# Performance work log

Hardware: AMD Instinct MI355X
Metric: run time of the kernel (lower is better)

## Reference

```python
import jax, jax.numpy as jnp
import numpy as np

B, N, D, NS, ITERS = 16, 4096, 512, 16, 3
EPS = 1e-8
H = max(D, 128)  # hidden_dim = max(dim, hidden_dim)
SCALE = D ** -0.5
LN_EPS = 1e-5  # torch LayerNorm default


def _ln(x, g, b):
    mu = x.mean(-1, keepdims=True)
    var = ((x - mu) ** 2).mean(-1, keepdims=True)
    return (x - mu) / jnp.sqrt(var + LN_EPS) * g + b


def setup_inputs() -> dict:
    key = jax.random.key(0)
    ks = jax.random.split(key, 16)
    s = 0.02
    return {
        "inputs": jax.random.normal(ks[0], (B, N, D), jnp.float32),
        "q_inp": jax.random.normal(ks[1], (B, N, D), jnp.float32),
        "k_inp": jax.random.normal(ks[2], (B, N, D), jnp.float32),
        "v_inp": jax.random.normal(ks[3], (B, N, D), jnp.float32),
        "slots_mu": jax.random.normal(ks[4], (1, NS, D), jnp.float32),
        "prompts": jax.random.uniform(ks[5], (1, NS, D), jnp.float32),
        "Wq": jax.random.normal(ks[6], (D, D), jnp.float32) * s,
        "bq": jnp.zeros((D,), jnp.float32),
        "W_ih": jax.random.normal(ks[7], (3 * D, D), jnp.float32) * s,
        "b_ih": jnp.zeros((3 * D,), jnp.float32),
        "W_hh": jax.random.normal(ks[8], (3 * D, D), jnp.float32) * s,
        "b_hh": jnp.zeros((3 * D,), jnp.float32),
        "W1": jax.random.normal(ks[9], (H, D), jnp.float32) * s,
        "b1": jnp.zeros((H,), jnp.float32),
        "W2": jax.random.normal(ks[10], (D, H), jnp.float32) * s,
        "b2": jnp.zeros((D,), jnp.float32),
        "gk": jnp.ones((D,), jnp.float32), "bk": jnp.zeros((D,), jnp.float32),
        "gv": jnp.ones((D,), jnp.float32), "bv": jnp.zeros((D,), jnp.float32),
        "gs": jnp.ones((D,), jnp.float32), "bs": jnp.zeros((D,), jnp.float32),
        "gff": jnp.ones((D,), jnp.float32), "bff": jnp.zeros((D,), jnp.float32),
    }


def reference(inputs, q_inp, k_inp, v_inp, slots_mu, prompts, Wq, bq,
              W_ih, b_ih, W_hh, b_hh, W1, b1, W2, b2,
              gk, bk, gv, bv, gs, bs, gff, bff):
    b = inputs.shape[0]
    slots = jnp.broadcast_to(slots_mu, (b, NS, D))
    prm = jnp.broadcast_to(prompts, (b, NS, D))
    k = _ln(k_inp, gk, bk)
    v = _ln(v_inp, gv, bv)

    attn = None
    for _ in range(ITERS):
        slots_prev = slots
        s = _ln(slots, gs, bs)
        q = jnp.einsum('bnd,ed->bne', s, Wq) + bq
        dots = jnp.einsum('bid,bjd->bij', q, k) * SCALE
        attn = jax.nn.softmax(dots, axis=1) + EPS  # inverted softmax over slots
        attn_n = attn / attn.sum(-1, keepdims=True)
        updates = jnp.einsum('bjd,bij->bid', v, attn_n)
        # GRUCell (torch semantics: gates order r, z, n)
        x = updates.reshape(-1, D)
        h = slots_prev.reshape(-1, D)
        gx = x @ W_ih.T + b_ih
        gh = h @ W_hh.T + b_hh
        rx, zx, nx = jnp.split(gx, 3, axis=-1)
        rh, zh, nh = jnp.split(gh, 3, axis=-1)
        r = jax.nn.sigmoid(rx + rh)
        z = jax.nn.sigmoid(zx + zh)
        n_t = jnp.tanh(nx + r * nh)
        slots = ((1.0 - z) * n_t + z * h).reshape(b, NS, D)
        ff = _ln(slots, gff, bff)
        slots = slots + (jax.nn.relu(ff @ W1.T + b1) @ W2.T + b2)

    # torch: einsum('bnd,bnp->bdp', ...).permute(0,2,1) == 'bnd,bnp->bpd'
    prompt_feature = jnp.einsum('bnd,bnp->bpd', prm, attn)
    slot_feature = jnp.einsum('bnd,bnp->bpd', slots, attn)
    return (slots, attn, prompt_feature, slot_feature, slot_feature)
```

## Files before the change

### kernel.cpp

```cpp
#include <hip/hip_runtime.h>
#include <math.h>

#define NN 4096
#define DD 512
#define NSL 16
#define SCALE_F 0.044194173824159216f
#define LN_EPS_F 1e-5f
#define ATTN_EPS_F 1e-8f

typedef float4 f4;
typedef __fp16 h2 __attribute__((ext_vector_type(2)));
typedef _Float16 h2f __attribute__((ext_vector_type(2)));
typedef _Float16 h8 __attribute__((ext_vector_type(8)));
typedef float f32x4 __attribute__((ext_vector_type(4)));

__device__ __forceinline__ float dot4f(f4 a, f4 b){
    return a.x*b.x + a.y*b.y + a.z*b.z + a.w*b.w;
}
__device__ __forceinline__ float fdot2u(unsigned a, unsigned b, float c){
    return __builtin_amdgcn_fdot2(__builtin_bit_cast(h2f, a),
                                  __builtin_bit_cast(h2f, b), c, false);
}
__device__ __forceinline__ unsigned pk(float x, float y){
    return __builtin_bit_cast(unsigned, __builtin_amdgcn_cvt_pkrtz(x, y));
}

__global__ __launch_bounds__(256) void k_prep(const float* __restrict__ mu,
        const float* __restrict__ kin, const float* __restrict__ vin,
        float* __restrict__ slots, __fp16* __restrict__ slotsh,
        float* __restrict__ kmu, float* __restrict__ krstd,
        float* __restrict__ vmu, float* __restrict__ vrstd,
        __fp16* __restrict__ kh, __fp16* __restrict__ vh,
        const float* __restrict__ Wq, const float* __restrict__ Wih,
        const float* __restrict__ Whh, const float* __restrict__ W1,
        const float* __restrict__ W2,
        uint2* __restrict__ TWq, uint2* __restrict__ TWih, uint2* __restrict__ TWhh,
        uint2* __restrict__ TW1, uint2* __restrict__ TW2){
    int bx = blockIdx.x, t = threadIdx.x;
    int gid = bx*256 + t;
    if (bx < 128){
        int idx = gid;
        f4 v = ((const f4*)mu)[idx & 2047];
        ((f4*)slots)[idx] = v;
        uint2 o; o.x = pk(v.x, v.y); o.y = pk(v.z, v.w);
        ((uint2*)slotsh)[idx] = o;
    }
    int sub = t & 15;
    int rl  = t >> 4;
#pragma unroll
    for (int pass = 0; pass < 8; pass++){
        int task = bx*128 + pass*16 + rl;
        int half = task >> 16;
        int row  = task & 65535;
        const float* src = half ? kin : vin;
        __fp16* dsth = half ? kh : vh;
        const f4* r4 = (const f4*)(src + (size_t)row*DD);
        uint2* w2 = (uint2*)(dsth + (size_t)row*DD);
        float s = 0.f, ss = 0.f;
#pragma unroll
        for (int k2 = 0; k2 < 8; k2++){
            f4 x = r4[sub + k2*16];
            s  += x.x+x.y+x.z+x.w;
            ss += x.x*x.x+x.y*x.y+x.z*x.z+x.w*x.w;
            uint2 o; o.x = pk(x.x, x.y); o.y = pk(x.z, x.w);
            w2[sub + k2*16] = o;
        }
        for (int o = 1; o < 16; o <<= 1){
            s += __shfl_xor(s, o); ss += __shfl_xor(ss, o);
        }
        if (sub == 0){
            float m = s*(1.f/DD);
            float rs = rsqrtf(ss*(1.f/DD) - m*m + LN_EPS_F);
            if (half){ kmu[row] = m; krstd[row] = rs; }
            else     { vmu[row] = m; vrstd[row] = rs; }
        }
    }
    for (int id = gid; id < 589824; id += 262144){
        const float* W; uint2* TW; int R, local;
        if (id < 65536)      { W = Wq;  TW = TWq;  R = 512;  local = id; }
        else if (id < 262144){ W = Wih; TW = TWih; R = 1536; local = id - 65536; }
        else if (id < 458752){ W = Whh; TW = TWhh; R = 1536; local = id - 262144; }
        else if (id < 524288){ W = W1;  TW = TW1;  R = 512;  local = id - 458752; }
        else                 { W = W2;  TW = TW2;  R = 512;  local = id - 524288; }
        int kk = local / R, c = local - kk*R;
        f4 w = ((const f4*)W)[(size_t)c*128 + kk];
        uint2 o; o.x = pk(w.x, w.y); o.y = pk(w.z, w.w);
        TW[local] = o;
    }
}

__global__ __launch_bounds__(256) void k_ln_q(const float* __restrict__ slots,
        const float* __restrict__ gs, const float* __restrict__ bs,
        const uint2* __restrict__ TWq, const float* __restrict__ bq,
        const float* __restrict__ gk, const float* __restrict__ bk,
        __fp16* __restrict__ qgh, float* __restrict__ C1p, float* __restrict__ C2p){
    __shared__ uint2 rowh[4][128];
    int lane = threadIdx.x & 63, wv = threadIdx.x >> 6;
    int m = blockIdx.y*4 + wv;
    int c = blockIdx.x*64 + lane;
    const f4* r4 = (const f4*)(slots + (size_t)m*DD);
    f4 v0 = r4[lane*2], v1 = r4[lane*2+1];
    float s  = v0.x+v0.y+v0.z+v0.w + v1.x+v1.y+v1.z+v1.w;
    float ss = v0.x*v0.x+v0.y*v0.y+v0.z*v0.z+v0.w*v0.w
             + v1.x*v1.x+v1.y*v1.y+v1.z*v1.z+v1.w*v1.w;
    for (int o = 32; o; o >>= 1){ s += __shfl_down(s,o); ss += __shfl_down(ss,o); }
    s = __shfl(s,0); ss = __shfl(ss,0);
    float mu = s*(1.f/DD);
    float rstd = rsqrtf(ss*(1.f/DD) - mu*mu + LN_EPS_F);
    const f4* g4 = (const f4*)gs; const f4* b4 = (const f4*)bs;
    f4 g0 = g4[lane*2], g1 = g4[lane*2+1], c0 = b4[lane*2], c1 = b4[lane*2+1];
    f4 o0, o1;
    o0.x=(v0.x-mu)*rstd*g0.x+c0.x; o0.y=(v0.y-mu)*rstd*g0.y+c0.y;
    o0.z=(v0.z-mu)*rstd*g0.z+c0.z; o0.w=(v0.w-mu)*rstd*g0.w+c0.w;
    o1.x=(v1.x-mu)*rstd*g1.x+c1.x; o1.y=(v1.y-mu)*rstd*g1.y+c1.y;
    o1.z=(v1.z-mu)*rstd*g1.z+c1.z; o1.w=(v1.w-mu)*rstd*g1.w+c1.w;
    rowh[wv][lane*2]     = uint2{pk(o0.x,o0.y), pk(o0.z,o0.w)};
    rowh[wv][lane*2 + 1] = uint2{pk(o1.x,o1.y), pk(o1.z,o1.w)};
    __syncthreads();
    float acc = 0.f;
    for (int kk = 0; kk < 128; kk++){
        uint2 q2 = rowh[wv][kk];
        uint2 w2 = TWq[(size_t)kk*512 + c];
        acc = fdot2u(w2.x, q2.x, acc);
        acc = fdot2u(w2.y, q2.y, acc);
    }
    float q0 = acc + bq[c];
    float qg0 = q0 * gk[c];
    float qg1 = __shfl_down(qg0, 1);
    if (!(lane & 1))
        ((unsigned*)qgh)[(size_t)m*256 + (c>>1)] = pk(qg0, qg1);
    float r1 = qg0, r2 = q0 * bk[c];
    for (int o = 32; o; o >>= 1){ r1 += __shfl_down(r1,o); r2 += __shfl_down(r2,o); }
    if (lane == 0){
        C1p[blockIdx.x*256 + m] = r1;
        C2p[blockIdx.x*256 + m] = r2;
    }
}

__global__ __launch_bounds__(256, 4) void k_attn_av(const __fp16* __restrict__ kh,
        const __fp16* __restrict__ vh, const __fp16* __restrict__ qgh,
        const float* __restrict__ C1p, const float* __restrict__ C2p,
        const float* __restrict__ kmu, const float* __restrict__ krstd,
        const float* __restrict__ vmu, const float* __restrict__ vrstd,
        float* __restrict__ Sp, float* __restrict__ Mp, __fp16* __restrict__ Uwp,
        float* __restrict__ attn_out, int last){
    __shared__ __align__(16) unsigned qLr[16*260];
    __shared__ __align__(16) unsigned wLp[32*20];
    __shared__ float c1s[NSL], c2s[NSL];
    __shared__ float kmuL[64], krsL[64], vmuL[64], vrsL[64];
    __shared__ float spL[4][NSL], mpL[4][NSL];
    int chunk = blockIdx.x, b = blockIdx.y;
    int t = threadIdx.x, lane = t & 63, wv = t >> 6;

    const unsigned* qsrc = (const unsigned*)(qgh + (size_t)b*NSL*DD);
    for (int e = t; e < 4096; e += 256)
        qLr[(e >> 8)*260 + (e & 255)] = qsrc[e];
    if (t < NSL){
        float c1 = 0.f, c2 = 0.f;
#pragma unroll
        for (int k = 0; k < 8; k++){
            c1 += C1p[k*256 + b*NSL + t];
            c2 += C2p[k*256 + b*NSL + t];
        }
        c1s[t] = c1; c2s[t] = c2;
    }
    {
        int grp = t >> 6, j0 = t & 63;
        size_t gidx = (size_t)b*NN + chunk*64 + j0;
        if (grp == 0) kmuL[j0] = kmu[gidx];
        else if (grp == 1) krsL[j0] = krstd[gidx];
        else if (grp == 2) vmuL[j0] = vmu[gidx];
        else vrsL[j0] = vrstd[gidx];
    }
    __syncthreads();

    int i = lane & 15, g = lane >> 4;
    int jbase = chunk*64 + wv*16;
    const uint4* ka = (const uint4*)(kh + ((size_t)b*NN + jbase + i)*DD);
    const uint4* qb4 = (const uint4*)qLr;
    f32x4 acc = {0.f, 0.f, 0.f, 0.f};
#pragma unroll
    for (int ks = 0; ks < 16; ks++){
        uint4 af = ka[ks*4 + g];
        uint4 bf = qb4[i*65 + ks*4 + g];
        acc = __builtin_amdgcn_mfma_f32_16x16x32_f16(
                  __builtin_bit_cast(h8, af), __builtin_bit_cast(h8, bf), acc, 0, 0, 0);
    }
    float c1i = c1s[i], c2i = c2s[i];
    float a4[4], w4v[4];
    float S_part = 0.f, M_part = 0.f;
#pragma unroll
    for (int r = 0; r < 4; r++){
        int jl = g*4 + r;
        float mu = kmuL[wv*16 + jl], rstd = krsL[wv*16 + jl];
        float dv = SCALE_F*(rstd*(acc[r] - mu*c1i) + c2i);
        float mx = dv;
        mx = fmaxf(mx, __shfl_xor(mx, 1));
        mx = fmaxf(mx, __shfl_xor(mx, 2));
        mx = fmaxf(mx, __shfl_xor(mx, 4));
        mx = fmaxf(mx, __shfl_xor(mx, 8));
        float e = __expf(dv - mx);
        float se = e;
        se += __shfl_xor(se, 1);
        se += __shfl_xor(se, 2);
        se += __shfl_xor(se, 4);
        se += __shfl_xor(se, 8);
        float a = e/se + ATTN_EPS_F;
        a4[r] = a;
        float rv = vrsL[wv*16 + jl], vm = vmuL[wv*16 + jl];
        w4v[r] = a*rv;
        S_part += a;
        M_part += a*rv*vm;
    }
    wLp[(wv*8 + g*2)*20 + i]     = pk(w4v[0], w4v[1]);
    wLp[(wv*8 + g*2 + 1)*20 + i] = pk(w4v[2], w4v[3]);
    S_part += __shfl_xor(S_part, 16);
    S_part += __shfl_xor(S_part, 32);
    M_part += __shfl_xor(M_part, 16);
    M_part += __shfl_xor(M_part, 32);
    if (lane < 16){ spL[wv][lane] = S_part; mpL[wv][lane] = M_part; }
    if (last){
#pragma unroll
        for (int r = 0; r < 4; r++)
            attn_out[((size_t)b*NSL + i)*NN + jbase + g*4 + r] = a4[r];
    }
    __syncthreads();

    if (t < NSL)
        Sp[((size_t)b*NSL + t)*64 + chunk] = spL[0][t]+spL[1][t]+spL[2][t]+spL[3][t];
    else if (t < 2*NSL){
        int ii = t - NSL;
        Mp[((size_t)b*NSL + ii)*64 + chunk] = mpL[0][ii]+mpL[1][ii]+mpL[2][ii]+mpL[3][ii];
    }

    f4 ax[4], ay[4];
#pragma unroll
    for (int g2 = 0; g2 < 4; g2++){ ax[g2] = f4{0,0,0,0}; ay[g2] = f4{0,0,0,0}; }
    const unsigned* v2h = (const unsigned*)(vh + ((size_t)b*NN + (size_t)chunk*64)*DD);
#pragma unroll 2
    for (int p = 0; p < 32; p++){
        unsigned vu0 = v2h[(size_t)(2*p)*256 + t];
        unsigned vu1 = v2h[(size_t)(2*p+1)*256 + t];
        unsigned pd0 = __builtin_amdgcn_perm(vu1, vu0, 0x05040100u);
        unsigned pd1 = __builtin_amdgcn_perm(vu1, vu0, 0x07060302u);
        const uint4* wp4 = (const uint4*)(wLp + p*20);
#pragma unroll
        for (int g2 = 0; g2 < 4; g2++){
            uint4 w = wp4[g2];
            ax[g2].x = fdot2u(w.x, pd0, ax[g2].x);
            ax[g2].y = fdot2u(w.y, pd0, ax[g2].y);
            ax[g2].z = fdot2u(w.z, pd0, ax[g2].z);
            ax[g2].w = fdot2u(w.w, pd0, ax[g2].w);
            ay[g2].x = fdot2u(w.x, pd1, ay[g2].x);
            ay[g2].y = fdot2u(w.y, pd1, ay[g2].y);
            ay[g2].z = fdot2u(w.z, pd1, ay[g2].z);
            ay[g2].w = fdot2u(w.w, pd1, ay[g2].w);
        }
    }
#pragma unroll
    for (int g2 = 0; g2 < 4; g2++){
        const float* px = (const float*)&ax[g2];
        const float* py = (const float*)&ay[g2];
#pragma unroll
        for (int c4 = 0; c4 < 4; c4++){
            int ii = g2*4 + c4;
            ((unsigned*)Uwp)[(((size_t)(b*NSL + ii))*64 + chunk)*256 + t] = pk(px[c4], py[c4]);
        }
    }
}

__global__ __launch_bounds__(256) void k_upd(const __fp16* __restrict__ Uwp,
        const float* __restrict__ Sp, const float* __restrict__ Mp,
        const float* __restrict__ gv, const float* __restrict__ bv,
        __fp16* __restrict__ updh){
    __shared__ float sm[2];
    int m = blockIdx.x, t = threadIdx.x;
    if (t < 128){
        float val = (t < 64) ? Sp[(size_t)m*64 + (t&63)] : Mp[(size_t)m*64 + (t&63)];
        for (int o = 1; o < 64; o <<= 1) val += __shfl_xor(val, o);
        if (t == 0)  sm[0] = val;
        if (t == 64) sm[1] = val;
    }
    __syncthreads();
    float Sv = sm[0], Mv = sm[1];
    float rS = 1.f/Sv;
    float accx = 0.f, accy = 0.f;
    const unsigned* base = (const unsigned*)Uwp + (size_t)m*64*256 + t;
#pragma unroll 8
    for (int ch = 0; ch < 64; ch++){
        h2 u = __builtin_bit_cast(h2, base[(size_t)ch*256]);
        accx += (float)u.x; accy += (float)u.y;
    }
    float2 gvv = ((const float2*)gv)[t];
    float2 bvv = ((const float2*)bv)[t];
    float ox = gvv.x*(accx - Mv)*rS + bvv.x;
    float oy = gvv.y*(accy - Mv)*rS + bvv.y;
    ((unsigned*)updh)[(size_t)m*256 + t] = pk(ox, oy);
}

__global__ __launch_bounds__(256) void k_gru_mm(const __fp16* __restrict__ xh, const __fp16* __restrict__ hh,
        const uint2* __restrict__ TWih, const float* __restrict__ bih,
        const uint2* __restrict__ TWhh, const float* __restrict__ bhh,
        float* __restrict__ gpA, float* __restrict__ gpB){
    int lane = threadIdx.x & 63, wv = threadIdx.x >> 6;
    int c = blockIdx.x*64 + lane;
    int m0 = blockIdx.y*16 + wv*4;
    int ks = blockIdx.z;
    int k0 = ks*64, k1 = k0 + 64;
    float* gp = ks ? gpB : gpA;
    int type = c >> 9;
    const uint2* x2 = (const uint2*)xh;
    const uint2* h2_ = (const uint2*)hh;
    float acc[4] = {0,0,0,0};
    float bias;
    if (type <= 1){
#pragma unroll 2
        for (int kk = k0; kk < k1; kk++){
            uint2 wa = TWih[(size_t)kk*1536 + c];
            uint2 wb = TWhh[(size_t)kk*1536 + c];
#pragma unroll
            for (int mm = 0; mm < 4; mm++){
                uint2 xa = x2[(size_t)(m0+mm)*128 + kk];
                uint2 ha = h2_[(size_t)(m0+mm)*128 + kk];
                acc[mm] = fdot2u(wa.x, xa.x, acc[mm]);
                acc[mm] = fdot2u(wa.y, xa.y, acc[mm]);
                acc[mm] = fdot2u(wb.x, ha.x, acc[mm]);
                acc[mm] = fdot2u(wb.y, ha.y, acc[mm]);
            }
        }
        bias = bih[c] + bhh[c];
    } else if (type == 2){
#pragma unroll 2
        for (int kk = k0; kk < k1; kk++){
            uint2 wa = TWih[(size_t)kk*1536 + c];
#pragma unroll
            for (int mm = 0; mm < 4; mm++){
                uint2 xa = x2[(size_t)(m0+mm)*128 + kk];
                acc[mm] = fdot2u(wa.x, xa.x, acc[mm]);
                acc[mm] = fdot2u(wa.y, xa.y, acc[mm]);
            }
        }
        bias = bih[c];
    } else {
        int cr = c - 512;
#pragma unroll 2
        for (int kk = k0; kk < k1; kk++){
            uint2 wb = TWhh[(size_t)kk*1536 + cr];
#pragma unroll
            for (int mm = 0; mm < 4; mm++){
                uint2 ha = h2_[(size_t)(m0+mm)*128 + kk];
                acc[mm] = fdot2u(wb.x, ha.x, acc[mm]);
                acc[mm] = fdot2u(wb.y, ha.y, acc[mm]);
            }
        }
        bias = bhh[cr];
    }
    float bout = ks ? 0.f : bias;
#pragma unroll
    for (int mm = 0; mm < 4; mm++)
        gp[(size_t)(m0+mm)*2048 + c] = acc[mm] + bout;
}

__global__ __launch_bounds__(256) void k_tail1(const float* __restrict__ gpA,
        const float* __restrict__ gpB, const float* __restrict__ slots,
        const float* __restrict__ gff, const float* __restrict__ bff,
        const uint2* __restrict__ TW1, const float* __restrict__ b1,
        float* __restrict__ slots2, __fp16* __restrict__ hidh){
    __shared__ uint2 rowh[4][128];
    int lane = threadIdx.x & 63, wv = threadIdx.x >> 6;
    int m = blockIdx.y*4 + wv;
    int c = blockIdx.x*64 + lane;
    const f4* g0 = (const f4*)(gpA + (size_t)m*2048);
    const f4* g1 = (const f4*)(gpB + (size_t)m*2048);
    const f4* h4 = (const f4*)(slots + (size_t)m*DD);
    f4 s2v[2];
    float s = 0.f, ss = 0.f;
#pragma unroll
    for (int half = 0; half < 2; half++){
        int e = lane*2 + half;
        f4 rp = g0[e],      zp = g0[128+e],  nx = g0[256+e],  nh = g0[384+e];
        f4 rq = g1[e],      zq = g1[128+e],  ny = g1[256+e],  nz = g1[384+e];
        rp.x+=rq.x; rp.y+=rq.y; rp.z+=rq.z; rp.w+=rq.w;
        zp.x+=zq.x; zp.y+=zq.y; zp.z+=zq.z; zp.w+=zq.w;
        nx.x+=ny.x; nx.y+=ny.y; nx.z+=ny.z; nx.w+=ny.w;
        nh.x+=nz.x; nh.y+=nz.y; nh.z+=nz.z; nh.w+=nz.w;
        f4 hv = h4[e];
        f4 o;
        {
            float r = 1.f/(1.f + __expf(-rp.x));
            float z = 1.f/(1.f + __expf(-zp.x));
            float n = tanhf(nx.x + r*nh.x);
            o.x = (1.f - z)*n + z*hv.x;
            r = 1.f/(1.f + __expf(-rp.y)); z = 1.f/(1.f + __expf(-zp.y));
            n = tanhf(nx.y + r*nh.y);
            o.y = (1.f - z)*n + z*hv.y;
            r = 1.f/(1.f + __expf(-rp.z)); z = 1.f/(1.f + __expf(-zp.z));
            n = tanhf(nx.z + r*nh.z);
            o.z = (1.f - z)*n + z*hv.z;
            r = 1.f/(1.f + __expf(-rp.w)); z = 1.f/(1.f + __expf(-zp.w));
            n = tanhf(nx.w + r*nh.w);
            o.w = (1.f - z)*n + z*hv.w;
        }
        s2v[half] = o;
        s  += o.x+o.y+o.z+o.w;
        ss += o.x*o.x+o.y*o.y+o.z*o.z+o.w*o.w;
        if (blockIdx.x == 0)
            ((f4*)(slots2 + (size_t)m*DD))[e] = o;
    }
    for (int o = 32; o; o >>= 1){ s += __shfl_down(s,o); ss += __shfl_down(ss,o); }
    s = __shfl(s,0); ss = __shfl(ss,0);
    float mu = s*(1.f/DD);
    float rstd = rsqrtf(ss*(1.f/DD) - mu*mu + LN_EPS_F);
    const f4* gg4 = (const f4*)gff; const f4* bb4 = (const f4*)bff;
#pragma unroll
    for (int half = 0; half < 2; half++){
        int e = lane*2 + half;
        f4 gg = gg4[e], bb = bb4[e], o = s2v[half], n;
        n.x = (o.x-mu)*rstd*gg.x + bb.x;
        n.y = (o.y-mu)*rstd*gg.y + bb.y;
        n.z = (o.z-mu)*rstd*gg.z + bb.z;
        n.w = (o.w-mu)*rstd*gg.w + bb.w;
        rowh[wv][e] = uint2{pk(n.x,n.y), pk(n.z,n.w)};
    }
    __syncthreads();
    float acc = 0.f;
    for (int kk = 0; kk < 128; kk++){
        uint2 q2 = rowh[wv][kk];
        uint2 w2 = TW1[(size_t)kk*512 + c];
        acc = fdot2u(w2.x, q2.x, acc);
        acc = fdot2u(w2.y, q2.y, acc);
    }
    float hv = fmaxf(acc + b1[c], 0.f);
    hidh[(size_t)m*DD + c] = (__fp16)hv;
}

__global__ __launch_bounds__(256) void k_ffn2(const __fp16* __restrict__ hidh, const uint2* __restrict__ TW2,
                                              const float* __restrict__ b2, const float* __restrict__ slots2,
                                              float* __restrict__ slots, __fp16* __restrict__ slotsh,
                                              float* __restrict__ out_slots, int last){
    int lane = threadIdx.x & 63, wv = threadIdx.x >> 6;
    int d = blockIdx.x*64 + lane;
    int m = blockIdx.y*4 + wv;
    const uint2* h2_ = (const uint2*)(hidh + (size_t)m*DD);
    float acc = 0.f;
    for (int kk = 0; kk < 128; kk++){
        uint2 hh = h2_[kk];
        uint2 w2 = TW2[(size_t)kk*512 + d];
        acc = fdot2u(w2.x, hh.x, acc);
        acc = fdot2u(w2.y, hh.y, acc);
    }
    float v0 = slots2[(size_t)m*DD + d] + acc + b2[d];
    slots[(size_t)m*DD + d] = v0;
    slotsh[(size_t)m*DD + d] = (__fp16)v0;
    if (last) out_slots[(size_t)m*DD + d] = v0;
}

__global__ __launch_bounds__(256) void k_features(const float* __restrict__ prompts, const float* __restrict__ slots,
        const float* __restrict__ attn, float* __restrict__ pf, float* __restrict__ sf, float* __restrict__ sf2){
    int b = blockIdx.y;
    int pbase = blockIdx.x*32;
    int t = threadIdx.x;
    __shared__ float al[NSL][33];
    for (int idx = t; idx < NSL*32; idx += 256){
        int i = idx >> 5, pp = idx & 31;
        al[i][pp] = attn[((size_t)b*NSL + i)*NN + pbase + pp];
    }
    float2 pr[NSL], sl[NSL];
    const float2* p2 = (const float2*)prompts;
    const float2* s2 = (const float2*)(slots + (size_t)b*NSL*DD);
#pragma unroll
    for (int i = 0; i < NSL; i++){ pr[i] = p2[i*256+t]; sl[i] = s2[i*256+t]; }
    __syncthreads();
    for (int pp = 0; pp < 32; pp++){
        float a0=0.f, a1=0.f, c0=0.f, c1=0.f;
#pragma unroll
        for (int i = 0; i < NSL; i++){
            float a = al[i][pp];
            a0 += a*pr[i].x; a1 += a*pr[i].y;
            c0 += a*sl[i].x; c1 += a*sl[i].y;
        }
        size_t o = ((size_t)b*NN + pbase + pp)*DD + 2*t;
        float2 pv; pv.x=a0; pv.y=a1;
        float2 sv; sv.x=c0; sv.y=c1;
        *(float2*)(pf + o)  = pv;
        *(float2*)(sf + o)  = sv;
        *(float2*)(sf2 + o) = sv;
    }
}

extern "C" void kernel_launch(void* const* d_in, const int* in_sizes, int n_in,
                              void* d_out, int out_size, void* d_ws, size_t ws_size,
                              hipStream_t stream) {
    const float* k_inp   = (const float*)d_in[2];
    const float* v_inp   = (const float*)d_in[3];
    const float* slots_mu= (const float*)d_in[4];
    const float* prompts = (const float*)d_in[5];
    const float* Wq      = (const float*)d_in[6];
    const float* bq      = (const float*)d_in[7];
    const float* W_ih    = (const float*)d_in[8];
    const float* b_ih    = (const float*)d_in[9];
    const float* W_hh    = (const float*)d_in[10];
    const float* b_hh    = (const float*)d_in[11];
    const float* W1      = (const float*)d_in[12];
    const float* b1      = (const float*)d_in[13];
    const float* W2      = (const float*)d_in[14];
    const float* b2      = (const float*)d_in[15];
    const float* gk      = (const float*)d_in[16];
    const float* bk      = (const float*)d_in[17];
    const float* gv      = (const float*)d_in[18];
    const float* bv      = (const float*)d_in[19];
    const float* gs      = (const float*)d_in[20];
    const float* bs      = (const float*)d_in[21];
    const float* gff     = (const float*)d_in[22];
    const float* bff     = (const float*)d_in[23];

    float* ws = (float*)d_ws;
    float* slots   = ws + 0;
    float* slots2  = ws + 131072;
    float* gp      = ws + 262144;
    float* C1p     = ws + 786432;
    float* C2p     = ws + 788480;
    float* kmu     = ws + 790528;
    float* krstd   = ws + 856064;
    float* vmu     = ws + 921600;
    float* vrstd   = ws + 987136;
    float* Sp      = ws + 1052672;
    float* Mp      = ws + 1069056;
    __fp16* slotsh = (__fp16*)(ws + 1085440);
    __fp16* updh   = (__fp16*)(ws + 1150976);
    __fp16* hidh   = (__fp16*)(ws + 1216512);
    __fp16* qgh    = (__fp16*)(ws + 1282048);
    uint2* TWqh  = (uint2*)(ws + 1347584);
    uint2* TWihh = (uint2*)(ws + 1478656);
    uint2* TWhhh = (uint2*)(ws + 1871872);
    uint2* TW1h  = (uint2*)(ws + 2265088);
    uint2* TW2h  = (uint2*)(ws + 2396160);

    float* out      = (float*)d_out;
    float* attn_out = out + 131072;
    float* pf       = out + 1179648;
    float* sf       = pf + 33554432;
    float* sf2      = sf + 33554432;
    __fp16* Uwp     = (__fp16*)pf;
    float* gpB      = pf + 16777216;
    __fp16* kh      = (__fp16*)sf;
    __fp16* vh      = (__fp16*)sf2;

    k_prep<<<1024, 256, 0, stream>>>(slots_mu, k_inp, v_inp, slots, slotsh,
                                     kmu, krstd, vmu, vrstd, kh, vh,
                                     Wq, W_ih, W_hh, W1, W2,
                                     TWqh, TWihh, TWhhh, TW1h, TW2h);

    for (int it = 0; it < 3; it++){
        int last = (it == 2);
        k_ln_q<<<dim3(8,64), 256, 0, stream>>>(slots, gs, bs, TWqh, bq, gk, bk, qgh, C1p, C2p);
        k_attn_av<<<dim3(64,16), 256, 0, stream>>>(kh, vh, qgh, C1p, C2p,
                                                   kmu, krstd, vmu, vrstd,
                                                   Sp, Mp, Uwp, attn_out, last);
        k_upd<<<256, 256, 0, stream>>>(Uwp, Sp, Mp, gv, bv, updh);
        k_gru_mm<<<dim3(32,16,2), 256, 0, stream>>>(updh, slotsh, TWihh, b_ih, TWhhh, b_hh, gp, gpB);
        k_tail1<<<dim3(8,64), 256, 0, stream>>>(gp, gpB, slots, gff, bff, TW1h, b1, slots2, hidh);
        k_ffn2<<<dim3(8,64), 256, 0, stream>>>(hidh, TW2h, b2, slots2, slots, slotsh, out, last);
    }

    k_features<<<dim3(128,16), 256, 0, stream>>>(prompts, slots, attn_out, pf, sf, sf2);
}
```

Before: 558.3 us.

## Fuse GRU tail, FFN and next-iteration LN+Q projection into one kernel

Merges k_tail1, k_ffn2 and the following iteration's k_ln_q into a single per-slot-row kernel with 512 threads. Intermediates (normalized rows, hidden activations) stay in LDS, and the slots2/hidh round trips through global memory go away. The first iteration's query is computed once from slots_mu by a small kernel and broadcast to all batches. This saves launches per iteration, but each block now runs three serial 512-wide matvecs over only 256 blocks, which lowers parallelism.

```diff
diff --git a/kernel.cpp b/kernel.cpp
--- a/kernel.cpp
+++ b/kernel.cpp
@@ -89,57 +89,52 @@
     }
 }
 
-__global__ __launch_bounds__(256) void k_ln_q(const float* __restrict__ slots,
+__global__ __launch_bounds__(256) void k_q0(const float* __restrict__ mu_,
+        const float* __restrict__ Wq, const float* __restrict__ bq,
         const float* __restrict__ gs, const float* __restrict__ bs,
-        const uint2* __restrict__ TWq, const float* __restrict__ bq,
         const float* __restrict__ gk, const float* __restrict__ bk,
-        __fp16* __restrict__ qgh, float* __restrict__ C1p, float* __restrict__ C2p){
-    __shared__ uint2 rowh[4][128];
-    int lane = threadIdx.x & 63, wv = threadIdx.x >> 6;
-    int m = blockIdx.y*4 + wv;
-    int c = blockIdx.x*64 + lane;
-    const f4* r4 = (const f4*)(slots + (size_t)m*DD);
-    f4 v0 = r4[lane*2], v1 = r4[lane*2+1];
-    float s  = v0.x+v0.y+v0.z+v0.w + v1.x+v1.y+v1.z+v1.w;
-    float ss = v0.x*v0.x+v0.y*v0.y+v0.z*v0.z+v0.w*v0.w
-             + v1.x*v1.x+v1.y*v1.y+v1.z*v1.z+v1.w*v1.w;
+        __fp16* __restrict__ qgh, float* __restrict__ C1v, float* __restrict__ C2v){
+    __shared__ __align__(16) float rowF[512];
+    __shared__ float sm[16];
+    int i = blockIdx.x, t = threadIdx.x, lane = t & 63, wv = t >> 6;
+    float2 x = ((const float2*)(mu_ + (size_t)i*DD))[t];
+    float s = x.x + x.y, ss = x.x*x.x + x.y*x.y;
     for (int o = 32; o; o >>= 1){ s += __shfl_down(s,o); ss += __shfl_down(ss,o); }
-    s = __shfl(s,0); ss = __shfl(ss,0);
-    float mu = s*(1.f/DD);
-    float rstd = rsqrtf(ss*(1.f/DD) - mu*mu + LN_EPS_F);
-    const f4* g4 = (const f4*)gs; const f4* b4 = (const f4*)bs;
-    f4 g0 = g4[lane*2], g1 = g4[lane*2+1], c0 = b4[lane*2], c1 = b4[lane*2+1];
-    f4 o0, o1;
-    o0.x=(v0.x-mu)*rstd*g0.x+c0.x; o0.y=(v0.y-mu)*rstd*g0.y+c0.y;
-    o0.z=(v0.z-mu)*rstd*g0.z+c0.z; o0.w=(v0.w-mu)*rstd*g0.w+c0.w;
-    o1.x=(v1.x-mu)*rstd*g1.x+c1.x; o1.y=(v1.y-mu)*rstd*g1.y+c1.y;
-    o1.z=(v1.z-mu)*rstd*g1.z+c1.z; o1.w=(v1.w-mu)*rstd*g1.w+c1.w;
-    rowh[wv][lane*2]     = uint2{pk(o0.x,o0.y), pk(o0.z,o0.w)};
-    rowh[wv][lane*2 + 1] = uint2{pk(o1.x,o1.y), pk(o1.z,o1.w)};
-    __syncthreads();
-    float acc = 0.f;
-    for (int kk = 0; kk < 128; kk++){
-        uint2 q2 = rowh[wv][kk];
-        uint2 w2 = TWq[(size_t)kk*512 + c];
-        acc = fdot2u(w2.x, q2.x, acc);
-        acc = fdot2u(w2.y, q2.y, acc);
-    }
-    float q0 = acc + bq[c];
-    float qg0 = q0 * gk[c];
-    float qg1 = __shfl_down(qg0, 1);
-    if (!(lane & 1))
-        ((unsigned*)qgh)[(size_t)m*256 + (c>>1)] = pk(qg0, qg1);
-    float r1 = qg0, r2 = q0 * bk[c];
-    for (int o = 32; o; o >>= 1){ r1 += __shfl_down(r1,o); r2 += __shfl_down(r2,o); }
-    if (lane == 0){
-        C1p[blockIdx.x*256 + m] = r1;
-        C2p[blockIdx.x*256 + m] = r2;
+    if (lane == 0){ sm[wv] = s; sm[8+wv] = ss; }
+    __syncthreads();
+    s = sm[0]+sm[1]+sm[2]+sm[3]; ss = sm[8]+sm[9]+sm[10]+sm[11];
+    float mu = s*(1.f/DD), rstd = rsqrtf(ss*(1.f/DD) - mu*mu + LN_EPS_F);
+    rowF[2*t]   = (x.x-mu)*rstd*gs[2*t]   + bs[2*t];
+    rowF[2*t+1] = (x.y-mu)*rstd*gs[2*t+1] + bs[2*t+1];
+    __syncthreads();
+    float c1p = 0.f, c2p = 0.f;
+#pragma unroll
+    for (int rep = 0; rep < 2; rep++){
+        int c = t + rep*256;
+        const f4* wrow = (const f4*)(Wq + (size_t)c*DD);
+        const f4* rf = (const f4*)rowF;
+        float acc = 0.f;
+        for (int k = 0; k < 128; k++) acc += dot4f(rf[k], wrow[k]);
+        float q0 = acc + bq[c];
+        float qg = q0 * gk[c];
+        __fp16 qh = (__fp16)qg;
+        for (int b = 0; b < 16; b++)
+            qgh[((size_t)(b*16+i))*DD + c] = qh;
+        c1p += qg; c2p += q0*bk[c];
+    }
+    for (int o = 32; o; o >>= 1){ c1p += __shfl_down(c1p,o); c2p += __shfl_down(c2p,o); }
+    if (lane == 0){ sm[wv] = c1p; sm[8+wv] = c2p; }
+    __syncthreads();
+    if (t == 0){
+        float r1 = sm[0]+sm[1]+sm[2]+sm[3];
+        float r2 = sm[8]+sm[9]+sm[10]+sm[11];
+        for (int b = 0; b < 16; b++){ C1v[b*16+i] = r1; C2v[b*16+i] = r2; }
     }
 }
 
 __global__ __launch_bounds__(256, 4) void k_attn_av(const __fp16* __restrict__ kh,
         const __fp16* __restrict__ vh, const __fp16* __restrict__ qgh,
-        const float* __restrict__ C1p, const float* __restrict__ C2p,
+        const float* __restrict__ C1v, const float* __restrict__ C2v,
         const float* __restrict__ kmu, const float* __restrict__ krstd,
         const float* __restrict__ vmu, const float* __restrict__ vrstd,
         float* __restrict__ Sp, float* __restrict__ Mp, __fp16* __restrict__ Uwp,
@@ -155,15 +150,7 @@
     const unsigned* qsrc = (const unsigned*)(qgh + (size_t)b*NSL*DD);
     for (int e = t; e < 4096; e += 256)
         qLr[(e >> 8)*260 + (e & 255)] = qsrc[e];
-    if (t < NSL){
-        float c1 = 0.f, c2 = 0.f;
-#pragma unroll
-        for (int k = 0; k < 8; k++){
-            c1 += C1p[k*256 + b*NSL + t];
-            c2 += C2p[k*256 + b*NSL + t];
-        }
-        c1s[t] = c1; c2s[t] = c2;
-    }
+    if (t < NSL){ c1s[t] = C1v[b*NSL + t]; c2s[t] = C2v[b*NSL + t]; }
     {
         int grp = t >> 6, j0 = t & 63;
         size_t gidx = (size_t)b*NN + chunk*64 + j0;
@@ -361,98 +348,99 @@
         gp[(size_t)(m0+mm)*2048 + c] = acc[mm] + bout;
 }
 
-__global__ __launch_bounds__(256) void k_tail1(const float* __restrict__ gpA,
-        const float* __restrict__ gpB, const float* __restrict__ slots,
+__global__ __launch_bounds__(512) void k_tail(const float* __restrict__ gpA,
+        const float* __restrict__ gpB, float* __restrict__ slots,
         const float* __restrict__ gff, const float* __restrict__ bff,
         const uint2* __restrict__ TW1, const float* __restrict__ b1,
-        float* __restrict__ slots2, __fp16* __restrict__ hidh){
-    __shared__ uint2 rowh[4][128];
-    int lane = threadIdx.x & 63, wv = threadIdx.x >> 6;
-    int m = blockIdx.y*4 + wv;
-    int c = blockIdx.x*64 + lane;
-    const f4* g0 = (const f4*)(gpA + (size_t)m*2048);
-    const f4* g1 = (const f4*)(gpB + (size_t)m*2048);
-    const f4* h4 = (const f4*)(slots + (size_t)m*DD);
-    f4 s2v[2];
-    float s = 0.f, ss = 0.f;
-#pragma unroll
-    for (int half = 0; half < 2; half++){
-        int e = lane*2 + half;
-        f4 rp = g0[e],      zp = g0[128+e],  nx = g0[256+e],  nh = g0[384+e];
-        f4 rq = g1[e],      zq = g1[128+e],  ny = g1[256+e],  nz = g1[384+e];
-        rp.x+=rq.x; rp.y+=rq.y; rp.z+=rq.z; rp.w+=rq.w;
-        zp.x+=zq.x; zp.y+=zq.y; zp.z+=zq.z; zp.w+=zq.w;
-        nx.x+=ny.x; nx.y+=ny.y; nx.z+=ny.z; nx.w+=ny.w;
-        nh.x+=nz.x; nh.y+=nz.y; nh.z+=nz.z; nh.w+=nz.w;
-        f4 hv = h4[e];
-        f4 o;
-        {
-            float r = 1.f/(1.f + __expf(-rp.x));
-            float z = 1.f/(1.f + __expf(-zp.x));
-            float n = tanhf(nx.x + r*nh.x);
-            o.x = (1.f - z)*n + z*hv.x;
-            r = 1.f/(1.f + __expf(-rp.y)); z = 1.f/(1.f + __expf(-zp.y));
-            n = tanhf(nx.y + r*nh.y);
-            o.y = (1.f - z)*n + z*hv.y;
-            r = 1.f/(1.f + __expf(-rp.z)); z = 1.f/(1.f + __expf(-zp.z));
-            n = tanhf(nx.z + r*nh.z);
-            o.z = (1.f - z)*n + z*hv.z;
-            r = 1.f/(1.f + __expf(-rp.w)); z = 1.f/(1.f + __expf(-zp.w));
-            n = tanhf(nx.w + r*nh.w);
-            o.w = (1.f - z)*n + z*hv.w;
-        }
-        s2v[half] = o;
-        s  += o.x+o.y+o.z+o.w;
-        ss += o.x*o.x+o.y*o.y+o.z*o.z+o.w*o.w;
-        if (blockIdx.x == 0)
-            ((f4*)(slots2 + (size_t)m*DD))[e] = o;
-    }
+        const uint2* __restrict__ TW2, const float* __restrict__ b2,
+        const float* __restrict__ gs, const float* __restrict__ bs,
+        const uint2* __restrict__ TWq, const float* __restrict__ bq,
+        const float* __restrict__ gk, const float* __restrict__ bk,
+        __fp16* __restrict__ slotsh, __fp16* __restrict__ qgh,
+        float* __restrict__ C1v, float* __restrict__ C2v,
+        float* __restrict__ out_slots, int last){
+    __shared__ __align__(8) __fp16 rowL[512];
+    __shared__ __align__(8) __fp16 hidL[512];
+    __shared__ float sm[16];
+    int m = blockIdx.x, t = threadIdx.x;
+    int lane = t & 63, wv = t >> 6;
+    const float* g0 = gpA + (size_t)m*2048;
+    const float* g1 = gpB + (size_t)m*2048;
+    float rp  = g0[t]       + g1[t];
+    float zp  = g0[512+t]   + g1[512+t];
+    float nx  = g0[1024+t]  + g1[1024+t];
+    float nh_ = g0[1536+t]  + g1[1536+t];
+    float h = slots[(size_t)m*DD + t];
+    float r = 1.f/(1.f + __expf(-rp));
+    float z = 1.f/(1.f + __expf(-zp));
+    float n = tanhf(nx + r*nh_);
+    float s2 = (1.f - z)*n + z*h;
+    float s = s2, ss = s2*s2;
     for (int o = 32; o; o >>= 1){ s += __shfl_down(s,o); ss += __shfl_down(ss,o); }
-    s = __shfl(s,0); ss = __shfl(ss,0);
-    float mu = s*(1.f/DD);
-    float rstd = rsqrtf(ss*(1.f/DD) - mu*mu + LN_EPS_F);
-    const f4* gg4 = (const f4*)gff; const f4* bb4 = (const f4*)bff;
-#pragma unroll
-    for (int half = 0; half < 2; half++){
-        int e = lane*2 + half;
-        f4 gg = gg4[e], bb = bb4[e], o = s2v[half], n;
-        n.x = (o.x-mu)*rstd*gg.x + bb.x;
-        n.y = (o.y-mu)*rstd*gg.y + bb.y;
-        n.z = (o.z-mu)*rstd*gg.z + bb.z;
-        n.w = (o.w-mu)*rstd*gg.w + bb.w;
-        rowh[wv][e] = uint2{pk(n.x,n.y), pk(n.z,n.w)};
-    }
-    __syncthreads();
+    if (lane == 0){ sm[wv] = s; sm[8+wv] = ss; }
+    __syncthreads();
+    s  = sm[0]+sm[1]+sm[2]+sm[3]+sm[4]+sm[5]+sm[6]+sm[7];
+    ss = sm[8]+sm[9]+sm[10]+sm[11]+sm[12]+sm[13]+sm[14]+sm[15];
+    float mu = s*(1.f/DD), rstd = rsqrtf(ss*(1.f/DD) - mu*mu + LN_EPS_F);
+    __syncthreads();
+    rowL[t] = (__fp16)((s2-mu)*rstd*gff[t] + bff[t]);
+    __syncthreads();
+    const uint2* ffv = (const uint2*)rowL;
     float acc = 0.f;
+#pragma unroll 4
     for (int kk = 0; kk < 128; kk++){
-        uint2 q2 = rowh[wv][kk];
-        uint2 w2 = TW1[(size_t)kk*512 + c];
-        acc = fdot2u(w2.x, q2.x, acc);
-        acc = fdot2u(w2.y, q2.y, acc);
-    }
-    float hv = fmaxf(acc + b1[c], 0.f);
-    hidh[(size_t)m*DD + c] = (__fp16)hv;
-}
-
-__global__ __launch_bounds__(256) void k_ffn2(const __fp16* __restrict__ hidh, const uint2* __restrict__ TW2,
-                                              const float* __restrict__ b2, const float* __restrict__ slots2,
-                                              float* __restrict__ slots, __fp16* __restrict__ slotsh,
-                                              float* __restrict__ out_slots, int last){
-    int lane = threadIdx.x & 63, wv = threadIdx.x >> 6;
-    int d = blockIdx.x*64 + lane;
-    int m = blockIdx.y*4 + wv;
-    const uint2* h2_ = (const uint2*)(hidh + (size_t)m*DD);
-    float acc = 0.f;
+        uint2 w = TW1[(size_t)kk*512 + t];
+        uint2 q = ffv[kk];
+        acc = fdot2u(w.x, q.x, acc);
+        acc = fdot2u(w.y, q.y, acc);
+    }
+    hidL[t] = (__fp16)fmaxf(acc + b1[t], 0.f);
+    __syncthreads();
+    const uint2* hv = (const uint2*)hidL;
+    float acc2 = 0.f;
+#pragma unroll 4
     for (int kk = 0; kk < 128; kk++){
-        uint2 hh = h2_[kk];
-        uint2 w2 = TW2[(size_t)kk*512 + d];
-        acc = fdot2u(w2.x, hh.x, acc);
-        acc = fdot2u(w2.y, hh.y, acc);
-    }
-    float v0 = slots2[(size_t)m*DD + d] + acc + b2[d];
-    slots[(size_t)m*DD + d] = v0;
-    slotsh[(size_t)m*DD + d] = (__fp16)v0;
-    if (last) out_slots[(size_t)m*DD + d] = v0;
+        uint2 w = TW2[(size_t)kk*512 + t];
+        uint2 q = hv[kk];
+        acc2 = fdot2u(w.x, q.x, acc2);
+        acc2 = fdot2u(w.y, q.y, acc2);
+    }
+    float v0 = s2 + acc2 + b2[t];
+    slots[(size_t)m*DD + t] = v0;
+    slotsh[(size_t)m*DD + t] = (__fp16)v0;
+    if (last){
+        out_slots[(size_t)m*DD + t] = v0;
+        return;
+    }
+    float s3 = v0, ss3 = v0*v0;
+    for (int o = 32; o; o >>= 1){ s3 += __shfl_down(s3,o); ss3 += __shfl_down(ss3,o); }
+    if (lane == 0){ sm[wv] = s3; sm[8+wv] = ss3; }
+    __syncthreads();
+    s3  = sm[0]+sm[1]+sm[2]+sm[3]+sm[4]+sm[5]+sm[6]+sm[7];
+    ss3 = sm[8]+sm[9]+sm[10]+sm[11]+sm[12]+sm[13]+sm[14]+sm[15];
+    float mu2 = s3*(1.f/DD), rstd2 = rsqrtf(ss3*(1.f/DD) - mu2*mu2 + LN_EPS_F);
+    __syncthreads();
+    rowL[t] = (__fp16)((v0-mu2)*rstd2*gs[t] + bs[t]);
+    __syncthreads();
+    float accq = 0.f;
+#pragma unroll 4
+    for (int kk = 0; kk < 128; kk++){
+        uint2 w = TWq[(size_t)kk*512 + t];
+        uint2 q = ffv[kk];
+        accq = fdot2u(w.x, q.x, accq);
+        accq = fdot2u(w.y, q.y, accq);
+    }
+    float q0 = accq + bq[t];
+    float qg = q0 * gk[t];
+    qgh[(size_t)m*DD + t] = (__fp16)qg;
+    float c1 = qg, c2 = q0*bk[t];
+    for (int o = 32; o; o >>= 1){ c1 += __shfl_down(c1,o); c2 += __shfl_down(c2,o); }
+    if (lane == 0){ sm[wv] = c1; sm[8+wv] = c2; }
+    __syncthreads();
+    if (t == 0){
+        C1v[m] = sm[0]+sm[1]+sm[2]+sm[3]+sm[4]+sm[5]+sm[6]+sm[7];
+        C2v[m] = sm[8]+sm[9]+sm[10]+sm[11]+sm[12]+sm[13]+sm[14]+sm[15];
+    }
 }
 
 __global__ __launch_bounds__(256) void k_features(const float* __restrict__ prompts, const float* __restrict__ slots,
@@ -516,25 +504,23 @@
 
     float* ws = (float*)d_ws;
     float* slots   = ws + 0;
-    float* slots2  = ws + 131072;
-    float* gp      = ws + 262144;
-    float* C1p     = ws + 786432;
-    float* C2p     = ws + 788480;
-    float* kmu     = ws + 790528;
-    float* krstd   = ws + 856064;
-    float* vmu     = ws + 921600;
-    float* vrstd   = ws + 987136;
-    float* Sp      = ws + 1052672;
-    float* Mp      = ws + 1069056;
-    __fp16* slotsh = (__fp16*)(ws + 1085440);
-    __fp16* updh   = (__fp16*)(ws + 1150976);
-    __fp16* hidh   = (__fp16*)(ws + 1216512);
-    __fp16* qgh    = (__fp16*)(ws + 1282048);
-    uint2* TWqh  = (uint2*)(ws + 1347584);
-    uint2* TWihh = (uint2*)(ws + 1478656);
-    uint2* TWhhh = (uint2*)(ws + 1871872);
-    uint2* TW1h  = (uint2*)(ws + 2265088);
-    uint2* TW2h  = (uint2*)(ws + 2396160);
+    float* gp      = ws + 131072;
+    float* C1v     = ws + 655360;
+    float* C2v     = ws + 655616;
+    float* kmu     = ws + 655872;
+    float* krstd   = ws + 721408;
+    float* vmu     = ws + 786944;
+    float* vrstd   = ws + 852480;
+    float* Sp      = ws + 918016;
+    float* Mp      = ws + 934400;
+    __fp16* slotsh = (__fp16*)(ws + 950784);
+    __fp16* updh   = (__fp16*)(ws + 1016320);
+    __fp16* qgh    = (__fp16*)(ws + 1081856);
+    uint2* TWqh  = (uint2*)(ws + 1147392);
+    uint2* TWihh = (uint2*)(ws + 1278464);
+    uint2* TWhhh = (uint2*)(ws + 1671680);
+    uint2* TW1h  = (uint2*)(ws + 2064896);
+    uint2* TW2h  = (uint2*)(ws + 2195968);
 
     float* out      = (float*)d_out;
     float* attn_out = out + 131072;
@@ -550,17 +536,18 @@
                                      kmu, krstd, vmu, vrstd, kh, vh,
                                      Wq, W_ih, W_hh, W1, W2,
                                      TWqh, TWihh, TWhhh, TW1h, TW2h);
+    k_q0<<<16, 256, 0, stream>>>(slots_mu, Wq, bq, gs, bs, gk, bk, qgh, C1v, C2v);
 
     for (int it = 0; it < 3; it++){
         int last = (it == 2);
-        k_ln_q<<<dim3(8,64), 256, 0, stream>>>(slots, gs, bs, TWqh, bq, gk, bk, qgh, C1p, C2p);
-        k_attn_av<<<dim3(64,16), 256, 0, stream>>>(kh, vh, qgh, C1p, C2p,
+        k_attn_av<<<dim3(64,16), 256, 0, stream>>>(kh, vh, qgh, C1v, C2v,
                                                    kmu, krstd, vmu, vrstd,
                                                    Sp, Mp, Uwp, attn_out, last);
         k_upd<<<256, 256, 0, stream>>>(Uwp, Sp, Mp, gv, bv, updh);
         k_gru_mm<<<dim3(32,16,2), 256, 0, stream>>>(updh, slotsh, TWihh, b_ih, TWhhh, b_hh, gp, gpB);
-        k_tail1<<<dim3(8,64), 256, 0, stream>>>(gp, gpB, slots, gff, bff, TW1h, b1, slots2, hidh);
-        k_ffn2<<<dim3(8,64), 256, 0, stream>>>(hidh, TW2h, b2, slots2, slots, slotsh, out, last);
+        k_tail<<<256, 512, 0, stream>>>(gp, gpB, slots, gff, bff, TW1h, b1, TW2h, b2,
+                                        gs, bs, TWqh, bq, gk, bk,
+                                        slotsh, qgh, C1v, C2v, out, last);
     }
 
     k_features<<<dim3(128,16), 256, 0, stream>>>(prompts, slots, attn_out, pf, sf, sf2);
```

Measured after the change: 576.6 us. +3.3%, slower.

## Fuse slot LayerNorm and q projection into FFN2 tail kernel

Applied to the files above, without the earlier changes.

Removes the separate per-iteration LN+q kernel. The first-iteration q is now computed once from slots_mu, which is identical across batches, and broadcast to all batches. Later iterations compute q inside the FFN2 kernel, so each block recomputes the full 512-wide FFN2 row to get LayerNorm statistics before doing its 64-column q slice. This saves a launch and a global round-trip per iteration but makes each FFN2 block do eight times the FFN2 matvec work.

```diff
diff --git a/kernel.cpp b/kernel.cpp
--- a/kernel.cpp
+++ b/kernel.cpp
@@ -89,51 +89,53 @@
     }
 }
 
-__global__ __launch_bounds__(256) void k_ln_q(const float* __restrict__ slots,
+__global__ __launch_bounds__(256) void k_q0(const float* __restrict__ mu_,
+        const float* __restrict__ Wq, const float* __restrict__ bq,
         const float* __restrict__ gs, const float* __restrict__ bs,
-        const uint2* __restrict__ TWq, const float* __restrict__ bq,
         const float* __restrict__ gk, const float* __restrict__ bk,
         __fp16* __restrict__ qgh, float* __restrict__ C1p, float* __restrict__ C2p){
-    __shared__ uint2 rowh[4][128];
-    int lane = threadIdx.x & 63, wv = threadIdx.x >> 6;
-    int m = blockIdx.y*4 + wv;
-    int c = blockIdx.x*64 + lane;
-    const f4* r4 = (const f4*)(slots + (size_t)m*DD);
-    f4 v0 = r4[lane*2], v1 = r4[lane*2+1];
-    float s  = v0.x+v0.y+v0.z+v0.w + v1.x+v1.y+v1.z+v1.w;
-    float ss = v0.x*v0.x+v0.y*v0.y+v0.z*v0.z+v0.w*v0.w
-             + v1.x*v1.x+v1.y*v1.y+v1.z*v1.z+v1.w*v1.w;
+    __shared__ __align__(16) float rowF[512];
+    __shared__ float sm[16];
+    int i = blockIdx.x, t = threadIdx.x, lane = t & 63, wv = t >> 6;
+    float2 x = ((const float2*)(mu_ + (size_t)i*DD))[t];
+    float s = x.x + x.y, ss = x.x*x.x + x.y*x.y;
     for (int o = 32; o; o >>= 1){ s += __shfl_down(s,o); ss += __shfl_down(ss,o); }
-    s = __shfl(s,0); ss = __shfl(ss,0);
-    float mu = s*(1.f/DD);
-    float rstd = rsqrtf(ss*(1.f/DD) - mu*mu + LN_EPS_F);
-    const f4* g4 = (const f4*)gs; const f4* b4 = (const f4*)bs;
-    f4 g0 = g4[lane*2], g1 = g4[lane*2+1], c0 = b4[lane*2], c1 = b4[lane*2+1];
-    f4 o0, o1;
-    o0.x=(v0.x-mu)*rstd*g0.x+c0.x; o0.y=(v0.y-mu)*rstd*g0.y+c0.y;
-    o0.z=(v0.z-mu)*rstd*g0.z+c0.z; o0.w=(v0.w-mu)*rstd*g0.w+c0.w;
-    o1.x=(v1.x-mu)*rstd*g1.x+c1.x; o1.y=(v1.y-mu)*rstd*g1.y+c1.y;
-    o1.z=(v1.z-mu)*rstd*g1.z+c1.z; o1.w=(v1.w-mu)*rstd*g1.w+c1.w;
-    rowh[wv][lane*2]     = uint2{pk(o0.x,o0.y), pk(o0.z,o0.w)};
-    rowh[wv][lane*2 + 1] = uint2{pk(o1.x,o1.y), pk(o1.z,o1.w)};
-    __syncthreads();
-    float acc = 0.f;
-    for (int kk = 0; kk < 128; kk++){
-        uint2 q2 = rowh[wv][kk];
-        uint2 w2 = TWq[(size_t)kk*512 + c];
-        acc = fdot2u(w2.x, q2.x, acc);
-        acc = fdot2u(w2.y, q2.y, acc);
-    }
-    float q0 = acc + bq[c];
-    float qg0 = q0 * gk[c];
-    float qg1 = __shfl_down(qg0, 1);
-    if (!(lane & 1))
-        ((unsigned*)qgh)[(size_t)m*256 + (c>>1)] = pk(qg0, qg1);
-    float r1 = qg0, r2 = q0 * bk[c];
-    for (int o = 32; o; o >>= 1){ r1 += __shfl_down(r1,o); r2 += __shfl_down(r2,o); }
-    if (lane == 0){
-        C1p[blockIdx.x*256 + m] = r1;
-        C2p[blockIdx.x*256 + m] = r2;
+    if (lane == 0){ sm[wv] = s; sm[8+wv] = ss; }
+    __syncthreads();
+    s = sm[0]+sm[1]+sm[2]+sm[3]; ss = sm[8]+sm[9]+sm[10]+sm[11];
+    float mu = s*(1.f/DD), rstd = rsqrtf(ss*(1.f/DD) - mu*mu + LN_EPS_F);
+    rowF[2*t]   = (x.x-mu)*rstd*gs[2*t]   + bs[2*t];
+    rowF[2*t+1] = (x.y-mu)*rstd*gs[2*t+1] + bs[2*t+1];
+    __syncthreads();
+    float c1p = 0.f, c2p = 0.f;
+#pragma unroll
+    for (int rep = 0; rep < 2; rep++){
+        int c = t + rep*256;
+        const f4* wrow = (const f4*)(Wq + (size_t)c*DD);
+        const f4* rf = (const f4*)rowF;
+        float acc = 0.f;
+        for (int k = 0; k < 128; k++) acc += dot4f(rf[k], wrow[k]);
+        float q0 = acc + bq[c];
+        float qg = q0 * gk[c];
+        __fp16 qh = (__fp16)qg;
+        for (int b = 0; b < 16; b++)
+            qgh[((size_t)(b*16+i))*DD + c] = qh;
+        c1p += qg; c2p += q0*bk[c];
+    }
+    for (int o = 32; o; o >>= 1){ c1p += __shfl_down(c1p,o); c2p += __shfl_down(c2p,o); }
+    __syncthreads();
+    if (lane == 0){ sm[wv] = c1p; sm[8+wv] = c2p; }
+    __syncthreads();
+    if (t == 0){
+        float r1 = sm[0]+sm[1]+sm[2]+sm[3];
+        float r2 = sm[8]+sm[9]+sm[10]+sm[11];
+        for (int b = 0; b < 16; b++){
+            C1p[b*16+i] = r1; C2p[b*16+i] = r2;
+            for (int k = 1; k < 8; k++){
+                C1p[k*256 + b*16+i] = 0.f;
+                C2p[k*256 + b*16+i] = 0.f;
+            }
+        }
     }
 }
 
@@ -434,25 +436,84 @@
     hidh[(size_t)m*DD + c] = (__fp16)hv;
 }
 
-__global__ __launch_bounds__(256) void k_ffn2(const __fp16* __restrict__ hidh, const uint2* __restrict__ TW2,
-                                              const float* __restrict__ b2, const float* __restrict__ slots2,
-                                              float* __restrict__ slots, __fp16* __restrict__ slotsh,
-                                              float* __restrict__ out_slots, int last){
+__global__ __launch_bounds__(256) void k_ffn2q(const __fp16* __restrict__ hidh,
+        const uint2* __restrict__ TW2, const float* __restrict__ b2,
+        const float* __restrict__ slots2,
+        const float* __restrict__ gs, const float* __restrict__ bs,
+        const uint2* __restrict__ TWq, const float* __restrict__ bq,
+        const float* __restrict__ gk, const float* __restrict__ bk,
+        float* __restrict__ slots, __fp16* __restrict__ slotsh,
+        __fp16* __restrict__ qgh, float* __restrict__ C1p, float* __restrict__ C2p,
+        float* __restrict__ out_slots, int last){
+    __shared__ __align__(16) uint4 hidL[4][64];
+    __shared__ __align__(16) unsigned rowq[4][256];
     int lane = threadIdx.x & 63, wv = threadIdx.x >> 6;
-    int d = blockIdx.x*64 + lane;
+    int cc = blockIdx.x;
     int m = blockIdx.y*4 + wv;
-    const uint2* h2_ = (const uint2*)(hidh + (size_t)m*DD);
+    hidL[wv][lane] = ((const uint4*)(hidh + (size_t)m*DD))[lane];
+    __syncthreads();
+    const uint4* tw2v = (const uint4*)TW2;
+    const uint2* hrow = (const uint2*)&hidL[wv][0];
+    float2 v0[4];
+    float s = 0.f, ss = 0.f;
+#pragma unroll
+    for (int j = 0; j < 4; j++){
+        int p = lane + j*64;
+        float a0 = 0.f, a1 = 0.f;
+#pragma unroll 4
+        for (int kk = 0; kk < 128; kk++){
+            uint4 w = tw2v[(size_t)kk*256 + p];
+            uint2 hq = hrow[kk];
+            a0 = fdot2u(w.x, hq.x, a0);
+            a0 = fdot2u(w.y, hq.y, a0);
+            a1 = fdot2u(w.z, hq.x, a1);
+            a1 = fdot2u(w.w, hq.y, a1);
+        }
+        float2 sl2 = ((const float2*)(slots2 + (size_t)m*DD))[p];
+        float2 bb = ((const float2*)b2)[p];
+        float2 v; v.x = sl2.x + a0 + bb.x; v.y = sl2.y + a1 + bb.y;
+        v0[j] = v;
+        s += v.x + v.y; ss += v.x*v.x + v.y*v.y;
+    }
+    for (int o = 32; o; o >>= 1){ s += __shfl_down(s,o); ss += __shfl_down(ss,o); }
+    s = __shfl(s,0); ss = __shfl(ss,0);
+    float mu = s*(1.f/DD), rstd = rsqrtf(ss*(1.f/DD) - mu*mu + LN_EPS_F);
+    int jown = cc >> 1, half = cc & 1;
+#pragma unroll
+    for (int j = 0; j < 4; j++){
+        int p = lane + j*64;
+        float2 v = v0[j];
+        if (j == jown && (lane >> 5) == half){
+            ((float2*)(slots + (size_t)m*DD))[p] = v;
+            ((unsigned*)slotsh)[(size_t)m*256 + p] = pk(v.x, v.y);
+            if (last) ((float2*)(out_slots + (size_t)m*DD))[p] = v;
+        }
+        if (!last){
+            float2 gg = ((const float2*)gs)[p];
+            float2 bb = ((const float2*)bs)[p];
+            float nx_ = (v.x-mu)*rstd*gg.x + bb.x;
+            float ny_ = (v.y-mu)*rstd*gg.y + bb.y;
+            rowq[wv][p] = pk(nx_, ny_);
+        }
+    }
+    if (last) return;
+    __syncthreads();
+    int c = cc*64 + lane;
+    const uint2* rq = (const uint2*)&rowq[wv][0];
     float acc = 0.f;
+#pragma unroll 4
     for (int kk = 0; kk < 128; kk++){
-        uint2 hh = h2_[kk];
-        uint2 w2 = TW2[(size_t)kk*512 + d];
-        acc = fdot2u(w2.x, hh.x, acc);
-        acc = fdot2u(w2.y, hh.y, acc);
-    }
-    float v0 = slots2[(size_t)m*DD + d] + acc + b2[d];
-    slots[(size_t)m*DD + d] = v0;
-    slotsh[(size_t)m*DD + d] = (__fp16)v0;
-    if (last) out_slots[(size_t)m*DD + d] = v0;
+        uint2 w = TWq[(size_t)kk*512 + c];
+        uint2 q = rq[kk];
+        acc = fdot2u(w.x, q.x, acc);
+        acc = fdot2u(w.y, q.y, acc);
+    }
+    float q0 = acc + bq[c];
+    float qg = q0 * gk[c];
+    qgh[(size_t)m*DD + c] = (__fp16)qg;
+    float r1 = qg, r2 = q0*bk[c];
+    for (int o = 32; o; o >>= 1){ r1 += __shfl_down(r1,o); r2 += __shfl_down(r2,o); }
+    if (lane == 0){ C1p[cc*256 + m] = r1; C2p[cc*256 + m] = r2; }
 }
 
 __global__ __launch_bounds__(256) void k_features(const float* __restrict__ prompts, const float* __restrict__ slots,
@@ -550,17 +611,19 @@
                                      kmu, krstd, vmu, vrstd, kh, vh,
                                      Wq, W_ih, W_hh, W1, W2,
                                      TWqh, TWihh, TWhhh, TW1h, TW2h);
+    k_q0<<<16, 256, 0, stream>>>(slots_mu, Wq, bq, gs, bs, gk, bk, qgh, C1p, C2p);
 
     for (int it = 0; it < 3; it++){
         int last = (it == 2);
-        k_ln_q<<<dim3(8,64), 256, 0, stream>>>(slots, gs, bs, TWqh, bq, gk, bk, qgh, C1p, C2p);
         k_attn_av<<<dim3(64,16), 256, 0, stream>>>(kh, vh, qgh, C1p, C2p,
                                                    kmu, krstd, vmu, vrstd,
                                                    Sp, Mp, Uwp, attn_out, last);
         k_upd<<<256, 256, 0, stream>>>(Uwp, Sp, Mp, gv, bv, updh);
         k_gru_mm<<<dim3(32,16,2), 256, 0, stream>>>(updh, slotsh, TWihh, b_ih, TWhhh, b_hh, gp, gpB);
         k_tail1<<<dim3(8,64), 256, 0, stream>>>(gp, gpB, slots, gff, bff, TW1h, b1, slots2, hidh);
-        k_ffn2<<<dim3(8,64), 256, 0, stream>>>(hidh, TW2h, b2, slots2, slots, slotsh, out, last);
+        k_ffn2q<<<dim3(8,64), 256, 0, stream>>>(hidh, TW2h, b2, slots2, gs, bs,
+                                                TWqh, bq, gk, bk,
+                                                slots, slotsh, qgh, C1p, C2p, out, last);
     }
 
     k_features<<<dim3(128,16), 256, 0, stream>>>(prompts, slots, attn_out, pf, sf, sf2);
```

Result: slower. 713.5 us (+27.8%).
